# Kernel optimization log

Measured on AMD Instinct MI355X. Metric: run time of the kernel, lower is better.

The kernel has to match this reference:

```python
import jax, jax.numpy as jnp
import numpy as np

N_QUBITS = 6
DIM = 2 ** N_QUBITS  # 64
Q_LAYERS = 2
CHUNK = 16

# ---- single-qubit rotation gate matrices (batched over leading dim) ----

def _rx(t):
    c = jnp.cos(t / 2).astype(jnp.complex64)
    s = jnp.sin(t / 2).astype(jnp.complex64)
    return jnp.stack([jnp.stack([c, -1j * s], -1), jnp.stack([-1j * s, c], -1)], -2)

def _ry(t):
    c = jnp.cos(t / 2).astype(jnp.complex64)
    s = jnp.sin(t / 2).astype(jnp.complex64)
    return jnp.stack([jnp.stack([c, -s], -1), jnp.stack([s, c], -1)], -2)

def _rz(t):
    e = jnp.exp(-0.5j * t.astype(jnp.complex64))
    z = jnp.zeros_like(e)
    return jnp.stack([jnp.stack([e, z], -1), jnp.stack([z, jnp.conj(e)], -1)], -2)


def _apply_1q(state, gate, wire):
    # state: (B, 64) complex64; gate: (B,2,2). PennyLane wire 0 = most-significant bit.
    dl, dr = 2 ** wire, 2 ** (N_QUBITS - 1 - wire)
    s = state.reshape(-1, dl, 2, dr)
    s = jnp.einsum('bkj,bljr->blkr', gate, s)
    return s.reshape(-1, DIM)


def _apply_crx(state, theta, control, target):
    s = state.reshape((-1,) + (2,) * N_QUBITS)
    s = jnp.moveaxis(s, (control + 1, target + 1), (1, 2))
    g = _rx(theta)  # (B,2,2)
    s1 = jnp.einsum('bkj,bj...->bk...', g, s[:, 1])
    s = jnp.concatenate([s[:, :1], s1[:, None]], axis=1)
    s = jnp.moveaxis(s, (1, 2), (control + 1, target + 1))
    return s.reshape(-1, DIM)


def _ansatz(state, params, n_layers):
    # unified ansatz: per layer, RX/RY/RZ on each qubit, ring of CRX forward, ring of CRX backward
    idx = 0
    for _ in range(n_layers):
        for i in range(N_QUBITS):
            state = _apply_1q(state, _rx(params[:, idx]), i)
            state = _apply_1q(state, _ry(params[:, idx + 1]), i)
            state = _apply_1q(state, _rz(params[:, idx + 2]), i)
            idx += 3
        for i in range(N_QUBITS):
            state = _apply_crx(state, params[:, idx], i, (i + 1) % N_QUBITS)
            idx += 1
        for i in range(N_QUBITS - 1, -1, -1):
            state = _apply_crx(state, params[:, idx], i, (i - 1) % N_QUBITS)
            idx += 1
    return state


_PX = jnp.array([[0, 1], [1, 0]], jnp.complex64)
_PY = jnp.array([[0, -1j], [1j, 0]], jnp.complex64)
_PZ = jnp.array([[1, 0], [0, -1]], jnp.complex64)


def _expvals(state):
    # expectations of X_i, Y_i, Z_i for all qubits -> (B, 3*n_qubits)
    outs = []
    B = state.shape[0]
    for P in (_PX, _PY, _PZ):
        g = jnp.broadcast_to(P, (B, 2, 2))
        for i in range(N_QUBITS):
            ps = _apply_1q(state, g, i)
            outs.append(jnp.sum(jnp.conj(state) * ps, axis=1).real)
    return jnp.stack(outs, axis=1).astype(jnp.float32)


def _forward(x, emb_w, emb_b, att_w1, att_b1, att_w2, att_b2, proj_w, proj_b,
             mix_re, mix_im, qff_params, out_w, out_b, ln_g, ln_b,
             cls_w1, cls_b1, cls_w2, cls_b2):
    B, C, T = x.shape
    # classical feature extractor: (B,C,T) -> (B,T,D)
    feats = jnp.einsum('bct,cd->btd', x, emb_w) + emb_b
    D = feats.shape[-1]
    n_chunks = T // CHUNK
    xc = feats.reshape(B, n_chunks, CHUNK, D)
    # attention-weighted chunk aggregation
    h = jnp.tanh(xc @ att_w1 + att_b1)
    scores = h @ att_w2 + att_b2                      # (B,nc,CHUNK,1)
    w = jax.nn.softmax(scores, axis=2)
    chunks = jnp.sum(w * xc, axis=2)                  # (B,nc,D)
    # quantum attention core: per-chunk ansatz params
    params = jax.nn.sigmoid(chunks @ proj_w + proj_b)  # (B,nc,60)
    flat = params.reshape(B * n_chunks, -1)
    state0 = jnp.zeros((B * n_chunks, DIM), jnp.complex64).at[:, 0].set(1.0)
    evolved = _ansatz(state0, flat, Q_LAYERS).reshape(B, n_chunks, DIM)
    # LCU mixing
    coeffs = (mix_re + 1j * mix_im).astype(jnp.complex64)
    coeffs = coeffs / (jnp.abs(coeffs).sum() + 1e-8)
    mixed = jnp.einsum('bti,t->bi', evolved, coeffs)
    norms = jnp.linalg.norm(mixed, axis=1, keepdims=True)
    mixed = mixed / (norms + 1e-9)
    # quantum feed-forward (shared params) + multi-observable measurement
    qp = jnp.broadcast_to(qff_params, (B, qff_params.shape[0]))
    qstate = _ansatz(mixed, qp, 1)
    qfeat = _expvals(qstate)                          # (B,18)
    out = qfeat @ out_w + out_b                       # (B,D)
    # LayerNorm
    mu = out.mean(-1, keepdims=True)
    var = out.var(-1, keepdims=True)
    out = (out - mu) / jnp.sqrt(var + 1e-5) * ln_g + ln_b
    # classifier head
    h2 = jax.nn.relu(out @ cls_w1 + cls_b1)
    return h2 @ cls_w2 + cls_b2


def setup_inputs() -> dict:
    key = jax.random.key(0)
    ks = jax.random.split(key, 20)
    B, C, T, D = 128, 64, 2048, 256
    NC = T // CHUNK        # 128 chunks
    NCP = 5 * N_QUBITS * Q_LAYERS  # 60 circuit params
    def nrm(k, shape, scale=0.05):
        return jax.random.normal(k, shape, jnp.float32) * scale
    return {
        'x': jax.random.normal(ks[0], (B, C, T), jnp.float32),
        'emb_w': nrm(ks[1], (C, D)), 'emb_b': nrm(ks[2], (D,)),
        'att_w1': nrm(ks[3], (D, D // 2)), 'att_b1': nrm(ks[4], (D // 2,)),
        'att_w2': nrm(ks[5], (D // 2, 1)), 'att_b2': nrm(ks[6], (1,)),
        'proj_w': nrm(ks[7], (D, NCP)), 'proj_b': nrm(ks[8], (NCP,)),
        'mix_re': jax.random.uniform(ks[9], (NC,), jnp.float32),
        'mix_im': jax.random.uniform(ks[10], (NC,), jnp.float32),
        'qff_params': nrm(ks[11], (5 * N_QUBITS,), 0.1),
        'out_w': nrm(ks[12], (3 * N_QUBITS, D)), 'out_b': nrm(ks[13], (D,)),
        'ln_g': jnp.ones((D,), jnp.float32), 'ln_b': jnp.zeros((D,), jnp.float32),
        'cls_w1': nrm(ks[14], (D, D)), 'cls_b1': nrm(ks[15], (D,)),
        'cls_w2': nrm(ks[16], (D, 2)), 'cls_b2': nrm(ks[17], (2,)),
    }


def reference(x, emb_w, emb_b, att_w1, att_b1, att_w2, att_b2, proj_w, proj_b,
              mix_re, mix_im, qff_params, out_w, out_b, ln_g, ln_b,
              cls_w1, cls_b1, cls_w2, cls_b2):
    return _forward(x, emb_w, emb_b, att_w1, att_b1, att_w2, att_b2, proj_w, proj_b,
                    mix_re, mix_im, qff_params, out_w, out_b, ln_g, ln_b,
                    cls_w1, cls_b1, cls_w2, cls_b2)
```

## Files before the change

kernel.cpp:

```cpp
#include <hip/hip_runtime.h>
#include <math.h>

#define NQ    6
#define QDIM  64
#define BB    128
#define CC    64
#define TT    2048
#define DD    256
#define NCH   128
#define CHLEN 16
#define HH    128
#define NCP   60

typedef __bf16 bf16x8 __attribute__((ext_vector_type(8)));
typedef float  f32x4  __attribute__((ext_vector_type(4)));

__device__ __forceinline__ float fast_tanh(float x) {
  float e = __expf(2.f * x);
  return 1.f - 2.f / (e + 1.f);
}

__device__ __forceinline__ float wave_sum(float v) {
#pragma unroll
  for (int off = 32; off >= 1; off >>= 1) v += __shfl_xor(v, off, 64);
  return v;
}

__device__ __forceinline__ void g_rx(float& re, float& im, int lane, int m, float half) {
  float c = __cosf(half), s = __sinf(half);
  float pre = __shfl_xor(re, m, 64);
  float pim = __shfl_xor(im, m, 64);
  float nre = c * re + s * pim;
  float nim = c * im - s * pre;
  re = nre; im = nim;
}
__device__ __forceinline__ void g_ry(float& re, float& im, int lane, int m, float half) {
  float c = __cosf(half), s = __sinf(half);
  float pre = __shfl_xor(re, m, 64);
  float pim = __shfl_xor(im, m, 64);
  float sg = (lane & m) ? s : -s;
  re = c * re + sg * pre;
  im = c * im + sg * pim;
}
__device__ __forceinline__ void g_rz(float& re, float& im, int lane, int m, float half) {
  float c = __cosf(half), s = __sinf(half);
  float sg = (lane & m) ? s : -s;
  float nre = c * re - sg * im;
  float nim = c * im + sg * re;
  re = nre; im = nim;
}
__device__ __forceinline__ void g_crx(float& re, float& im, int lane, int mc, int mt, float half) {
  float c = __cosf(half), s = __sinf(half);
  float pre = __shfl_xor(re, mt, 64);
  float pim = __shfl_xor(im, mt, 64);
  if (lane & mc) {
    float nre = c * re + s * pim;
    float nim = c * im - s * pre;
    re = nre; im = nim;
  }
}
__device__ __forceinline__ void ansatz_layer(float& re, float& im, int lane,
                                             const float* p) {
#pragma unroll
  for (int q = 0; q < 6; ++q) {
    int m = 1 << (5 - q);
    g_rx(re, im, lane, m, 0.5f * p[3 * q + 0]);
    g_ry(re, im, lane, m, 0.5f * p[3 * q + 1]);
    g_rz(re, im, lane, m, 0.5f * p[3 * q + 2]);
  }
#pragma unroll
  for (int q = 0; q < 6; ++q)
    g_crx(re, im, lane, 1 << (5 - q), 1 << (5 - ((q + 1) % 6)), 0.5f * p[18 + q]);
#pragma unroll
  for (int q = 5; q >= 0; --q)
    g_crx(re, im, lane, 1 << (5 - q), 1 << (5 - ((q + 5) % 6)), 0.5f * p[24 + (5 - q)]);
}

__global__ __launch_bounds__(256) void k0_prep(
    const float* __restrict__ emb_w, const float* __restrict__ emb_b,
    const float* __restrict__ att_w1, const float* __restrict__ att_b1,
    const float* __restrict__ proj_w, const float* __restrict__ proj_b,
    __bf16* __restrict__ WfH, __bf16* __restrict__ WfL,
    __bf16* __restrict__ PfH, __bf16* __restrict__ PfL,
    float* __restrict__ b_fused, float* __restrict__ pb_fused) {
  int idx = blockIdx.x * 256 + threadIdx.x;
  if (idx < 8192) {
    int j = idx & 127, k = idx >> 7;
    float a = 0.f;
    for (int d = 0; d < 256; ++d)
      a = fmaf(emb_w[k * 256 + d], att_w1[d * 128 + j], a);
    __bf16 h = (__bf16)a;
    WfH[j * 64 + k] = h; WfL[j * 64 + k] = (__bf16)(a - (float)h);
  } else if (idx < 12288) {
    int i = idx - 8192;
    int n = i & 63, k = i >> 6;
    float a = 0.f;
    if (n < 60)
      for (int d = 0; d < 256; ++d)
        a = fmaf(emb_w[k * 256 + d], proj_w[d * 60 + n], a);
    __bf16 h = (__bf16)a;
    PfH[n * 64 + k] = h; PfL[n * 64 + k] = (__bf16)(a - (float)h);
  } else if (idx < 12416) {
    int j = idx - 12288;
    float a = att_b1[j];
    for (int d = 0; d < 256; ++d) a = fmaf(emb_b[d], att_w1[d * 128 + j], a);
    b_fused[j] = a;
  } else if (idx < 12480) {
    int n = idx - 12416;
    float a = 0.f;
    if (n < 60) {
      a = proj_b[n];
      for (int d = 0; d < 256; ++d) a = fmaf(emb_b[d], proj_w[d * 60 + n], a);
    }
    pb_fused[n] = a;
  }
}

__global__ __launch_bounds__(256) void k1_fused(
    const float* __restrict__ x, const float* __restrict__ att_w2,
    const __bf16* __restrict__ WfH, const __bf16* __restrict__ WfL,
    const __bf16* __restrict__ PfH, const __bf16* __restrict__ PfL,
    const float* __restrict__ b_fused, const float* __restrict__ pb_fused,
    float2* __restrict__ evolved) {
  const int blk = blockIdx.x;
  const int b = blk >> 6, cp = blk & 63;
  const int tid = threadIdx.x, wv = tid >> 6, lane = tid & 63;
  const int l15 = lane & 15, quad = lane >> 4;

  __shared__ float xtile[32][68];
  __shared__ float scoreS[4][32];
  __shared__ float4 uniF4[512];
  char* uni = (char*)uniF4;
  bf16x8* afH = (bf16x8*)uni;
  bf16x8* afL = (bf16x8*)(uni + 4096);
  float*  wSm     = (float*)uni;
  __bf16* axH     = (__bf16*)(uni + 128);
  __bf16* axL     = (__bf16*)(uni + 384);
  float*  paramsS = (float*)(uni + 640);
  float4* matS    = (float4*)(uni + 1120);
  float2* crxS    = (float2*)(uni + 1888);

  {
#pragma unroll
    for (int pass = 0; pass < 2; ++pass) {
      int k = pass * 32 + (tid >> 3), t4 = tid & 7;
      float4 v = *(const float4*)(x + ((size_t)(b * 64 + k)) * 2048 + cp * 32 + t4 * 4);
      xtile[t4 * 4 + 0][k] = v.x; xtile[t4 * 4 + 1][k] = v.y;
      xtile[t4 * 4 + 2][k] = v.z; xtile[t4 * 4 + 3][k] = v.w;
    }
  }
  __syncthreads();

  {
    const int mt = tid >> 7, ks = (tid >> 6) & 1, ln = tid & 63;
    const float* src = &xtile[mt * 16 + (ln & 15)][ks * 32 + (ln >> 4) * 8];
    float4 u0 = *(const float4*)src, u1 = *(const float4*)(src + 4);
    float vals[8] = {u0.x, u0.y, u0.z, u0.w, u1.x, u1.y, u1.z, u1.w};
    bf16x8 h, l;
#pragma unroll
    for (int j = 0; j < 8; ++j) {
      __bf16 hh = (__bf16)vals[j];
      h[j] = hh;
      l[j] = (__bf16)(vals[j] - (float)hh);
    }
    afH[(mt * 2 + ks) * 64 + ln] = h;
    afL[(mt * 2 + ks) * 64 + ln] = l;
  }
  __syncthreads();

  f32x4 acc[2][2];
#pragma unroll
  for (int mt = 0; mt < 2; ++mt)
#pragma unroll
    for (int jt = 0; jt < 2; ++jt) acc[mt][jt] = (f32x4){0.f, 0.f, 0.f, 0.f};
#pragma unroll
  for (int mt = 0; mt < 2; ++mt) {
    bf16x8 ah[2], al[2];
#pragma unroll
    for (int ks = 0; ks < 2; ++ks) {
      ah[ks] = afH[(mt * 2 + ks) * 64 + lane];
      al[ks] = afL[(mt * 2 + ks) * 64 + lane];
    }
#pragma unroll
    for (int jt = 0; jt < 2; ++jt)
#pragma unroll
      for (int ks = 0; ks < 2; ++ks) {
        const size_t row = (size_t)(wv * 32 + jt * 16 + l15) * 64 + ks * 32 + 8 * quad;
        bf16x8 bh = *(const bf16x8*)(WfH + row);
        bf16x8 bl = *(const bf16x8*)(WfL + row);
        acc[mt][jt] = __builtin_amdgcn_mfma_f32_16x16x32_bf16(ah[ks], bh, acc[mt][jt], 0, 0, 0);
        acc[mt][jt] = __builtin_amdgcn_mfma_f32_16x16x32_bf16(al[ks], bh, acc[mt][jt], 0, 0, 0);
        acc[mt][jt] = __builtin_amdgcn_mfma_f32_16x16x32_bf16(ah[ks], bl, acc[mt][jt], 0, 0, 0);
      }
  }
  {
    float w2v[2], b1v[2];
#pragma unroll
    for (int jt = 0; jt < 2; ++jt) {
      int j = wv * 32 + jt * 16 + l15;
      w2v[jt] = att_w2[j];
      b1v[jt] = b_fused[j];
    }
#pragma unroll
    for (int mt = 0; mt < 2; ++mt)
#pragma unroll
      for (int r = 0; r < 4; ++r) {
        float sc = fast_tanh(acc[mt][0][r] + b1v[0]) * w2v[0] +
                   fast_tanh(acc[mt][1][r] + b1v[1]) * w2v[1];
        sc += __shfl_xor(sc, 1, 64);
        sc += __shfl_xor(sc, 2, 64);
        sc += __shfl_xor(sc, 4, 64);
        sc += __shfl_xor(sc, 8, 64);
        if (l15 == 0) scoreS[wv][mt * 16 + quad * 4 + r] = sc;
      }
  }
  __syncthreads();

  if (tid < 32) {
    const int c = tid >> 4, t = tid & 15, ct = c * 16 + t;
    float s = (scoreS[0][ct] + scoreS[1][ct]) + (scoreS[2][ct] + scoreS[3][ct]);
    float mx = s;
    mx = fmaxf(mx, __shfl_xor(mx, 1, 64));
    mx = fmaxf(mx, __shfl_xor(mx, 2, 64));
    mx = fmaxf(mx, __shfl_xor(mx, 4, 64));
    mx = fmaxf(mx, __shfl_xor(mx, 8, 64));
    float e = __expf(s - mx);
    float sum = e;
    sum += __shfl_xor(sum, 1, 64);
    sum += __shfl_xor(sum, 2, 64);
    sum += __shfl_xor(sum, 4, 64);
    sum += __shfl_xor(sum, 8, 64);
    wSm[ct] = e / sum;
  }
  __syncthreads();

  if (tid < 128) {
    const int c = tid >> 6, k = tid & 63;
    float a = 0.f;
#pragma unroll
    for (int t = 0; t < 16; ++t) a = fmaf(wSm[c * 16 + t], xtile[c * 16 + t][k], a);
    __bf16 h = (__bf16)a;
    axH[c * 64 + k] = h;
    axL[c * 64 + k] = (__bf16)(a - (float)h);
  }
  __syncthreads();

  {
    const int jout = wv * 16 + l15;
    f32x4 acc3 = (f32x4){0.f, 0.f, 0.f, 0.f};
#pragma unroll
    for (int ks = 0; ks < 2; ++ks) {
      const size_t row = (size_t)jout * 64 + ks * 32 + 8 * quad;
      bf16x8 bh = *(const bf16x8*)(PfH + row);
      bf16x8 bl = *(const bf16x8*)(PfL + row);
      bf16x8 ax = (bf16x8)(__bf16)0.f, alx = (bf16x8)(__bf16)0.f;
      if (l15 < 2) {
        ax  = *(const bf16x8*)(axH + l15 * 64 + ks * 32 + 8 * quad);
        alx = *(const bf16x8*)(axL + l15 * 64 + ks * 32 + 8 * quad);
      }
      acc3 = __builtin_amdgcn_mfma_f32_16x16x32_bf16(ax, bh, acc3, 0, 0, 0);
      acc3 = __builtin_amdgcn_mfma_f32_16x16x32_bf16(alx, bh, acc3, 0, 0, 0);
      acc3 = __builtin_amdgcn_mfma_f32_16x16x32_bf16(ax, bl, acc3, 0, 0, 0);
    }
    if (jout < 60 && quad == 0) {
      float pbias = pb_fused[jout];
      const int layer = (jout >= 30) ? 1 : 0;
      const int pm = jout - layer * 30;
#pragma unroll
      for (int r = 0; r < 2; ++r) {
        float a = acc3[r] + pbias;
        float p = 1.f / (1.f + __expf(-a));
        paramsS[r * 60 + jout] = p;
        if (pm >= 18) {
          float sn, cs;
          __sincosf(0.5f * p, &sn, &cs);
          crxS[r * 24 + layer * 12 + (pm - 18)] = make_float2(cs, sn);
        }
      }
    }
  }
  __syncthreads();

  if (tid < 24) {
    const int r = tid / 12, g = tid % 12;
    const float* pp = paramsS + r * 60 + (g / 6) * 30 + (g % 6) * 3;
    float sa, ca, sb, cb, sg, cg;
    __sincosf(0.5f * pp[0], &sa, &ca);
    __sincosf(0.5f * pp[1], &sb, &cb);
    __sincosf(0.5f * pp[2], &sg, &cg);
    float m00r = cb * ca, m00i = sb * sa;
    float m01r = -sb * ca, m01i = -cb * sa;
    float m10r = sb * ca, m10i = -cb * sa;
    float m11r = cb * ca, m11i = -sb * sa;
    float4 b0, b1;
    b0.x = cg * m00r + sg * m00i;  b0.y = cg * m00i - sg * m00r;
    b0.z = cg * m01r + sg * m01i;  b0.w = cg * m01i - sg * m01r;
    b1.x = cg * m11r - sg * m11i;  b1.y = cg * m11i + sg * m11r;
    b1.z = cg * m10r - sg * m10i;  b1.w = cg * m10i + sg * m10r;
    matS[(r * 12 + g) * 2 + 0] = b0;
    matS[(r * 12 + g) * 2 + 1] = b1;
  }
  __syncthreads();

  if (wv < 2) {
    float re = (lane == 0) ? 1.f : 0.f, im = 0.f;
    const float4* mats = matS + wv * 24;
    const float2* crxs = crxS + wv * 24;
#pragma unroll
    for (int l = 0; l < 2; ++l) {
#pragma unroll
      for (int q = 0; q < 6; ++q) {
        const int m = 1 << (5 - q);
        float4 M = mats[(l * 6 + q) * 2 + ((lane & m) ? 1 : 0)];
        float pre = __shfl_xor(re, m, 64);
        float pim = __shfl_xor(im, m, 64);
        float nre = M.x * re - M.y * im + M.z * pre - M.w * pim;
        float nim = M.x * im + M.y * re + M.z * pim + M.w * pre;
        re = nre; im = nim;
      }
#pragma unroll
      for (int e = 0; e < 12; ++e) {
        const int q = (e < 6) ? e : (11 - e);
        const int mc = 1 << (5 - q);
        const int mt = (e < 6) ? (1 << (5 - ((q + 1) % 6)))
                               : (1 << (5 - ((q + 5) % 6)));
        float2 cs = crxs[l * 12 + e];
        float pre = __shfl_xor(re, mt, 64);
        float pim = __shfl_xor(im, mt, 64);
        float nre = fmaf(cs.y, pim, cs.x * re);
        float nim = fmaf(-cs.y, pre, cs.x * im);
        bool act = (lane & mc) != 0;
        re = act ? nre : re;
        im = act ? nim : im;
      }
    }
    evolved[((size_t)b * NCH + cp * 2 + wv) * QDIM + lane] = make_float2(re, im);
  }
}

__global__ __launch_bounds__(512) void k3_head(
    const float2* __restrict__ evolved, const float* __restrict__ mix_re,
    const float* __restrict__ mix_im, const float* __restrict__ qff,
    const float* __restrict__ out_w, const float* __restrict__ out_b,
    const float* __restrict__ ln_g, const float* __restrict__ ln_b,
    const float* __restrict__ cls_w1, const float* __restrict__ cls_b1,
    const float* __restrict__ cls_w2, const float* __restrict__ cls_b2,
    float* __restrict__ outp) {
  const int b = blockIdx.x, tid = threadIdx.x, wv = tid >> 6, lane = tid & 63;
  __shared__ float mreS[8][64], mimS[8][64];
  __shared__ float qfeatS[18];
  __shared__ float outS[DD];
  __shared__ float redS[8];
  __shared__ float clsR[2][DD];

  float are = 0.f, aim = 0.f;
#pragma unroll 4
  for (int t = wv * 16; t < wv * 16 + 16; ++t) {
    float2 e = evolved[((size_t)b * NCH + t) * QDIM + lane];
    float cr = mix_re[t], ci = mix_im[t];
    are = fmaf(cr, e.x, are); are = fmaf(-ci, e.y, are);
    aim = fmaf(cr, e.y, aim); aim = fmaf(ci, e.x, aim);
  }
  mreS[wv][lane] = are; mimS[wv][lane] = aim;
  __syncthreads();

  if (wv == 0) {
    float r0 = mix_re[lane], i0 = mix_im[lane];
    float r1 = mix_re[lane + 64], i1 = mix_im[lane + 64];
    float sp = sqrtf(r0 * r0 + i0 * i0) + sqrtf(r1 * r1 + i1 * i1);
    float S = wave_sum(sp) + 1e-8f;
    float re = 0.f, im = 0.f;
#pragma unroll
    for (int w = 0; w < 8; ++w) { re += mreS[w][lane]; im += mimS[w][lane]; }
    float invS = 1.f / S;
    re *= invS; im *= invS;
    float n2 = wave_sum(re * re + im * im);
    float scl = 1.f / (sqrtf(n2) + 1e-9f);
    re *= scl; im *= scl;
    float qp[30];
#pragma unroll
    for (int i = 0; i < 30; ++i) qp[i] = qff[i];
    ansatz_layer(re, im, lane, qp);
#pragma unroll
    for (int q = 0; q < 6; ++q) {
      int m = 1 << (5 - q);
      float pre = __shfl_xor(re, m, 64), pim = __shfl_xor(im, m, 64);
      float vx = re * pre + im * pim;
      float vy = (lane & m) ? (im * pre - re * pim) : (re * pim - im * pre);
      float vz = (lane & m) ? -(re * re + im * im) : (re * re + im * im);
      vx = wave_sum(vx); vy = wave_sum(vy); vz = wave_sum(vz);
      if (lane == 0) { qfeatS[q] = vx; qfeatS[6 + q] = vy; qfeatS[12 + q] = vz; }
    }
  }
  __syncthreads();

  float o = 0.f, dv = 0.f;
  if (tid < 256) {
    o = out_b[tid];
#pragma unroll
    for (int k = 0; k < 18; ++k) o = fmaf(qfeatS[k], out_w[k * DD + tid], o);
    float s1 = wave_sum(o);
    if (lane == 0) redS[wv] = s1;
  }
  __syncthreads();
  float mu = (redS[0] + redS[1] + redS[2] + redS[3]) * (1.f / 256.f);
  if (tid < 256) {
    dv = o - mu;
    float s2 = wave_sum(dv * dv);
    if (lane == 0) redS[wv] = s2;
  }
  __syncthreads();
  float var = (redS[0] + redS[1] + redS[2] + redS[3]) * (1.f / 256.f);
  if (tid < 256) {
    outS[tid] = dv / sqrtf(var + 1e-5f) * ln_g[tid] + ln_b[tid];
  }
  __syncthreads();

  {
    const int dd = tid & 255, hh = tid >> 8;
    float r = (hh == 0) ? cls_b1[dd] : 0.f;
#pragma unroll 8
    for (int d = hh * 128; d < hh * 128 + 128; ++d)
      r = fmaf(outS[d], cls_w1[(size_t)d * DD + dd], r);
    clsR[hh][dd] = r;
  }
  __syncthreads();
  if (tid < 256) {
    float r = fmaxf(clsR[0][tid] + clsR[1][tid], 0.f);
    float p0 = wave_sum(r * cls_w2[tid * 2 + 0]);
    float p1 = wave_sum(r * cls_w2[tid * 2 + 1]);
    if (lane == 0) { mreS[0][wv] = p0; mreS[1][wv] = p1; }
  }
  __syncthreads();
  if (tid == 0) {
    outp[b * 2 + 0] = (mreS[0][0] + mreS[0][1]) + (mreS[0][2] + mreS[0][3]) + cls_b2[0];
    outp[b * 2 + 1] = (mreS[1][0] + mreS[1][1]) + (mreS[1][2] + mreS[1][3]) + cls_b2[1];
  }
}

extern "C" void kernel_launch(void* const* d_in, const int* in_sizes, int n_in,
                              void* d_out, int out_size, void* d_ws, size_t ws_size,
                              hipStream_t stream) {
  const float* x      = (const float*)d_in[0];
  const float* emb_w  = (const float*)d_in[1];
  const float* emb_b  = (const float*)d_in[2];
  const float* att_w1 = (const float*)d_in[3];
  const float* att_b1 = (const float*)d_in[4];
  const float* att_w2 = (const float*)d_in[5];
  const float* proj_w = (const float*)d_in[7];
  const float* proj_b = (const float*)d_in[8];
  const float* mix_re = (const float*)d_in[9];
  const float* mix_im = (const float*)d_in[10];
  const float* qff    = (const float*)d_in[11];
  const float* out_w  = (const float*)d_in[12];
  const float* out_b  = (const float*)d_in[13];
  const float* ln_g   = (const float*)d_in[14];
  const float* ln_b   = (const float*)d_in[15];
  const float* cls_w1 = (const float*)d_in[16];
  const float* cls_b1 = (const float*)d_in[17];
  const float* cls_w2 = (const float*)d_in[18];
  const float* cls_b2 = (const float*)d_in[19];

  char* ws = (char*)d_ws;
  float2* evolved = (float2*)ws;
  size_t off = 8388608;
  __bf16* WfH = (__bf16*)(ws + off); off += 16384;
  __bf16* WfL = (__bf16*)(ws + off); off += 16384;
  __bf16* PfH = (__bf16*)(ws + off); off += 8192;
  __bf16* PfL = (__bf16*)(ws + off); off += 8192;
  float* b_fused  = (float*)(ws + off); off += 512;
  float* pb_fused = (float*)(ws + off); off += 256;

  k0_prep<<<49, 256, 0, stream>>>(emb_w, emb_b, att_w1, att_b1, proj_w, proj_b,
                                  WfH, WfL, PfH, PfL, b_fused, pb_fused);
  k1_fused<<<BB * 64, 256, 0, stream>>>(
      x, att_w2, WfH, WfL, PfH, PfL, b_fused, pb_fused, evolved);
  k3_head<<<BB, 512, 0, stream>>>(evolved, mix_re, mix_im, qff, out_w, out_b,
                                  ln_g, ln_b, cls_w1, cls_b1, cls_w2, cls_b2,
                                  (float*)d_out);
}
```

Before: 211.0 us.

## Split prep dot products across 8 lanes; process four chunks per fused block

The prep kernel now splits each length-256 dot product across 8 threads and combines the partials with shuffles, launching 390 blocks instead of 49, so a serial per-thread reduction no longer dominates that kernel. The main fused kernel handles 64 timesteps (four chunks) per block instead of 32, halving the grid. Each WfH/WfL fragment loaded from memory now feeds four M-tiles, and all four waves run the quantum circuit instead of two. In exchange the fused kernel uses more shared memory and more accumulator registers, which can lower occupancy.

```diff
diff --git a/kernel.cpp b/kernel.cpp
--- a/kernel.cpp
+++ b/kernel.cpp
@@ -84,35 +84,58 @@
     __bf16* __restrict__ PfH, __bf16* __restrict__ PfL,
     float* __restrict__ b_fused, float* __restrict__ pb_fused) {
   int idx = blockIdx.x * 256 + threadIdx.x;
-  if (idx < 8192) {
-    int j = idx & 127, k = idx >> 7;
+  if (idx < 65536) {
+    int out = idx >> 3, part = idx & 7;
+    int j = out & 127, k = out >> 7;
+    int d0 = part * 32;
     float a = 0.f;
-    for (int d = 0; d < 256; ++d)
+#pragma unroll 8
+    for (int d = d0; d < d0 + 32; ++d)
       a = fmaf(emb_w[k * 256 + d], att_w1[d * 128 + j], a);
-    __bf16 h = (__bf16)a;
-    WfH[j * 64 + k] = h; WfL[j * 64 + k] = (__bf16)(a - (float)h);
-  } else if (idx < 12288) {
-    int i = idx - 8192;
-    int n = i & 63, k = i >> 6;
-    float a = 0.f;
-    if (n < 60)
-      for (int d = 0; d < 256; ++d)
-        a = fmaf(emb_w[k * 256 + d], proj_w[d * 60 + n], a);
-    __bf16 h = (__bf16)a;
-    PfH[n * 64 + k] = h; PfL[n * 64 + k] = (__bf16)(a - (float)h);
-  } else if (idx < 12416) {
-    int j = idx - 12288;
-    float a = att_b1[j];
-    for (int d = 0; d < 256; ++d) a = fmaf(emb_b[d], att_w1[d * 128 + j], a);
-    b_fused[j] = a;
-  } else if (idx < 12480) {
-    int n = idx - 12416;
+    a += __shfl_xor(a, 1, 64); a += __shfl_xor(a, 2, 64); a += __shfl_xor(a, 4, 64);
+    if (part == 0) {
+      __bf16 h = (__bf16)a;
+      WfH[j * 64 + k] = h; WfL[j * 64 + k] = (__bf16)(a - (float)h);
+    }
+  } else if (idx < 98304) {
+    int i2 = idx - 65536;
+    int out = i2 >> 3, part = i2 & 7;
+    int n = out & 63, k = out >> 6;
     float a = 0.f;
     if (n < 60) {
-      a = proj_b[n];
-      for (int d = 0; d < 256; ++d) a = fmaf(emb_b[d], proj_w[d * 60 + n], a);
-    }
-    pb_fused[n] = a;
+      int d0 = part * 32;
+#pragma unroll 8
+      for (int d = d0; d < d0 + 32; ++d)
+        a = fmaf(emb_w[k * 256 + d], proj_w[d * 60 + n], a);
+    }
+    a += __shfl_xor(a, 1, 64); a += __shfl_xor(a, 2, 64); a += __shfl_xor(a, 4, 64);
+    if (part == 0) {
+      __bf16 h = (__bf16)a;
+      PfH[n * 64 + k] = h; PfL[n * 64 + k] = (__bf16)(a - (float)h);
+    }
+  } else if (idx < 99328) {
+    int i3 = idx - 98304;
+    int out = i3 >> 3, part = i3 & 7;
+    float a = (part == 0) ? att_b1[out] : 0.f;
+    int d0 = part * 32;
+#pragma unroll 8
+    for (int d = d0; d < d0 + 32; ++d)
+      a = fmaf(emb_b[d], att_w1[d * 128 + out], a);
+    a += __shfl_xor(a, 1, 64); a += __shfl_xor(a, 2, 64); a += __shfl_xor(a, 4, 64);
+    if (part == 0) b_fused[out] = a;
+  } else if (idx < 99840) {
+    int i4 = idx - 99328;
+    int out = i4 >> 3, part = i4 & 7;
+    float a = 0.f;
+    if (out < 60) {
+      if (part == 0) a = proj_b[out];
+      int d0 = part * 32;
+#pragma unroll 8
+      for (int d = d0; d < d0 + 32; ++d)
+        a = fmaf(emb_b[d], proj_w[d * 60 + out], a);
+    }
+    a += __shfl_xor(a, 1, 64); a += __shfl_xor(a, 2, 64); a += __shfl_xor(a, 4, 64);
+    if (part == 0) pb_fused[out] = a;
   }
 }
 
@@ -123,28 +146,28 @@
     const float* __restrict__ b_fused, const float* __restrict__ pb_fused,
     float2* __restrict__ evolved) {
   const int blk = blockIdx.x;
-  const int b = blk >> 6, cp = blk & 63;
+  const int b = blk >> 5, cq = blk & 31;
   const int tid = threadIdx.x, wv = tid >> 6, lane = tid & 63;
   const int l15 = lane & 15, quad = lane >> 4;
 
-  __shared__ float xtile[32][68];
-  __shared__ float scoreS[4][32];
-  __shared__ float4 uniF4[512];
+  __shared__ float xtile[64][68];
+  __shared__ float scoreS[4][64];
+  __shared__ float4 uniF4[1024];
   char* uni = (char*)uniF4;
   bf16x8* afH = (bf16x8*)uni;
-  bf16x8* afL = (bf16x8*)(uni + 4096);
+  bf16x8* afL = (bf16x8*)(uni + 8192);
   float*  wSm     = (float*)uni;
-  __bf16* axH     = (__bf16*)(uni + 128);
-  __bf16* axL     = (__bf16*)(uni + 384);
-  float*  paramsS = (float*)(uni + 640);
-  float4* matS    = (float4*)(uni + 1120);
-  float2* crxS    = (float2*)(uni + 1888);
-
-  {
-#pragma unroll
-    for (int pass = 0; pass < 2; ++pass) {
-      int k = pass * 32 + (tid >> 3), t4 = tid & 7;
-      float4 v = *(const float4*)(x + ((size_t)(b * 64 + k)) * 2048 + cp * 32 + t4 * 4);
+  __bf16* axH     = (__bf16*)(uni + 256);
+  __bf16* axL     = (__bf16*)(uni + 768);
+  float*  paramsS = (float*)(uni + 1280);
+  float4* matS    = (float4*)(uni + 2240);
+  float2* crxS    = (float2*)(uni + 5312);
+
+  {
+#pragma unroll
+    for (int pass = 0; pass < 4; ++pass) {
+      int k = pass * 16 + (tid >> 4), t4 = tid & 15;
+      float4 v = *(const float4*)(x + ((size_t)(b * 64 + k)) * 2048 + cq * 64 + t4 * 4);
       xtile[t4 * 4 + 0][k] = v.x; xtile[t4 * 4 + 1][k] = v.y;
       xtile[t4 * 4 + 2][k] = v.z; xtile[t4 * 4 + 3][k] = v.w;
     }
@@ -152,46 +175,51 @@
   __syncthreads();
 
   {
-    const int mt = tid >> 7, ks = (tid >> 6) & 1, ln = tid & 63;
-    const float* src = &xtile[mt * 16 + (ln & 15)][ks * 32 + (ln >> 4) * 8];
-    float4 u0 = *(const float4*)src, u1 = *(const float4*)(src + 4);
-    float vals[8] = {u0.x, u0.y, u0.z, u0.w, u1.x, u1.y, u1.z, u1.w};
-    bf16x8 h, l;
-#pragma unroll
-    for (int j = 0; j < 8; ++j) {
-      __bf16 hh = (__bf16)vals[j];
-      h[j] = hh;
-      l[j] = (__bf16)(vals[j] - (float)hh);
-    }
-    afH[(mt * 2 + ks) * 64 + ln] = h;
-    afL[(mt * 2 + ks) * 64 + ln] = l;
-  }
-  __syncthreads();
-
-  f32x4 acc[2][2];
-#pragma unroll
-  for (int mt = 0; mt < 2; ++mt)
+#pragma unroll
+    for (int it = 0; it < 2; ++it) {
+      int item = it * 256 + tid;
+      int ln = item & 63, ks = (item >> 6) & 1, mt = item >> 7;
+      const float* src = &xtile[mt * 16 + (ln & 15)][ks * 32 + (ln >> 4) * 8];
+      float4 u0 = *(const float4*)src, u1 = *(const float4*)(src + 4);
+      float vals[8] = {u0.x, u0.y, u0.z, u0.w, u1.x, u1.y, u1.z, u1.w};
+      bf16x8 h, l;
+#pragma unroll
+      for (int j = 0; j < 8; ++j) {
+        __bf16 hh = (__bf16)vals[j];
+        h[j] = hh;
+        l[j] = (__bf16)(vals[j] - (float)hh);
+      }
+      afH[(mt * 2 + ks) * 64 + ln] = h;
+      afL[(mt * 2 + ks) * 64 + ln] = l;
+    }
+  }
+  __syncthreads();
+
+  f32x4 acc[4][2];
+#pragma unroll
+  for (int mt = 0; mt < 4; ++mt)
 #pragma unroll
     for (int jt = 0; jt < 2; ++jt) acc[mt][jt] = (f32x4){0.f, 0.f, 0.f, 0.f};
 #pragma unroll
-  for (int mt = 0; mt < 2; ++mt) {
-    bf16x8 ah[2], al[2];
-#pragma unroll
-    for (int ks = 0; ks < 2; ++ks) {
-      ah[ks] = afH[(mt * 2 + ks) * 64 + lane];
-      al[ks] = afL[(mt * 2 + ks) * 64 + lane];
-    }
-#pragma unroll
-    for (int jt = 0; jt < 2; ++jt)
-#pragma unroll
-      for (int ks = 0; ks < 2; ++ks) {
-        const size_t row = (size_t)(wv * 32 + jt * 16 + l15) * 64 + ks * 32 + 8 * quad;
-        bf16x8 bh = *(const bf16x8*)(WfH + row);
-        bf16x8 bl = *(const bf16x8*)(WfL + row);
-        acc[mt][jt] = __builtin_amdgcn_mfma_f32_16x16x32_bf16(ah[ks], bh, acc[mt][jt], 0, 0, 0);
-        acc[mt][jt] = __builtin_amdgcn_mfma_f32_16x16x32_bf16(al[ks], bh, acc[mt][jt], 0, 0, 0);
-        acc[mt][jt] = __builtin_amdgcn_mfma_f32_16x16x32_bf16(ah[ks], bl, acc[mt][jt], 0, 0, 0);
-      }
+  for (int ks = 0; ks < 2; ++ks) {
+    bf16x8 ah[4], al[4];
+#pragma unroll
+    for (int mt = 0; mt < 4; ++mt) {
+      ah[mt] = afH[(mt * 2 + ks) * 64 + lane];
+      al[mt] = afL[(mt * 2 + ks) * 64 + lane];
+    }
+#pragma unroll
+    for (int jt = 0; jt < 2; ++jt) {
+      const size_t row = (size_t)(wv * 32 + jt * 16 + l15) * 64 + ks * 32 + 8 * quad;
+      bf16x8 bh = *(const bf16x8*)(WfH + row);
+      bf16x8 bl = *(const bf16x8*)(WfL + row);
+#pragma unroll
+      for (int mt = 0; mt < 4; ++mt) {
+        acc[mt][jt] = __builtin_amdgcn_mfma_f32_16x16x32_bf16(ah[mt], bh, acc[mt][jt], 0, 0, 0);
+        acc[mt][jt] = __builtin_amdgcn_mfma_f32_16x16x32_bf16(al[mt], bh, acc[mt][jt], 0, 0, 0);
+        acc[mt][jt] = __builtin_amdgcn_mfma_f32_16x16x32_bf16(ah[mt], bl, acc[mt][jt], 0, 0, 0);
+      }
+    }
   }
   {
     float w2v[2], b1v[2];
@@ -202,7 +230,7 @@
       b1v[jt] = b_fused[j];
     }
 #pragma unroll
-    for (int mt = 0; mt < 2; ++mt)
+    for (int mt = 0; mt < 4; ++mt)
 #pragma unroll
       for (int r = 0; r < 4; ++r) {
         float sc = fast_tanh(acc[mt][0][r] + b1v[0]) * w2v[0] +
@@ -216,7 +244,7 @@
   }
   __syncthreads();
 
-  if (tid < 32) {
+  if (tid < 64) {
     const int c = tid >> 4, t = tid & 15, ct = c * 16 + t;
     float s = (scoreS[0][ct] + scoreS[1][ct]) + (scoreS[2][ct] + scoreS[3][ct]);
     float mx = s;
@@ -234,8 +262,8 @@
   }
   __syncthreads();
 
-  if (tid < 128) {
-    const int c = tid >> 6, k = tid & 63;
+  {
+    const int c = wv, k = lane;
     float a = 0.f;
 #pragma unroll
     for (int t = 0; t < 16; ++t) a = fmaf(wSm[c * 16 + t], xtile[c * 16 + t][k], a);
@@ -254,7 +282,7 @@
       bf16x8 bh = *(const bf16x8*)(PfH + row);
       bf16x8 bl = *(const bf16x8*)(PfL + row);
       bf16x8 ax = (bf16x8)(__bf16)0.f, alx = (bf16x8)(__bf16)0.f;
-      if (l15 < 2) {
+      if (l15 < 4) {
         ax  = *(const bf16x8*)(axH + l15 * 64 + ks * 32 + 8 * quad);
         alx = *(const bf16x8*)(axL + l15 * 64 + ks * 32 + 8 * quad);
       }
@@ -267,7 +295,7 @@
       const int layer = (jout >= 30) ? 1 : 0;
       const int pm = jout - layer * 30;
 #pragma unroll
-      for (int r = 0; r < 2; ++r) {
+      for (int r = 0; r < 4; ++r) {
         float a = acc3[r] + pbias;
         float p = 1.f / (1.f + __expf(-a));
         paramsS[r * 60 + jout] = p;
@@ -281,7 +309,7 @@
   }
   __syncthreads();
 
-  if (tid < 24) {
+  if (tid < 48) {
     const int r = tid / 12, g = tid % 12;
     const float* pp = paramsS + r * 60 + (g / 6) * 30 + (g % 6) * 3;
     float sa, ca, sb, cb, sg, cg;
@@ -302,7 +330,7 @@
   }
   __syncthreads();
 
-  if (wv < 2) {
+  {
     float re = (lane == 0) ? 1.f : 0.f, im = 0.f;
     const float4* mats = matS + wv * 24;
     const float2* crxs = crxS + wv * 24;
@@ -334,7 +362,7 @@
         im = act ? nim : im;
       }
     }
-    evolved[((size_t)b * NCH + cp * 2 + wv) * QDIM + lane] = make_float2(re, im);
+    evolved[((size_t)b * NCH + cq * 4 + wv) * QDIM + lane] = make_float2(re, im);
   }
 }
 
@@ -471,9 +499,9 @@
   float* b_fused  = (float*)(ws + off); off += 512;
   float* pb_fused = (float*)(ws + off); off += 256;
 
-  k0_prep<<<49, 256, 0, stream>>>(emb_w, emb_b, att_w1, att_b1, proj_w, proj_b,
-                                  WfH, WfL, PfH, PfL, b_fused, pb_fused);
-  k1_fused<<<BB * 64, 256, 0, stream>>>(
+  k0_prep<<<390, 256, 0, stream>>>(emb_w, emb_b, att_w1, att_b1, proj_w, proj_b,
+                                   WfH, WfL, PfH, PfL, b_fused, pb_fused);
+  k1_fused<<<BB * 32, 256, 0, stream>>>(
       x, att_w2, WfH, WfL, PfH, PfL, b_fused, pb_fused, evolved);
   k3_head<<<BB, 512, 0, stream>>>(evolved, mix_re, mix_im, qff, out_w, out_b,
                                   ln_g, ln_b, cls_w1, cls_b1, cls_w2, cls_b2,
```

Measured after the change: 203.9 us. 3.4% less time.
